# Kernel optimization log

Hardware: AMD Instinct MI355X
Metric: run time of the kernel (lower is better)

Reference implementation:

```python
import jax, jax.numpy as jnp
import numpy as np


def _layernorm(x, g, b, eps=1e-5):
    m = jnp.mean(x, axis=-1, keepdims=True)
    v = jnp.var(x, axis=-1, keepdims=True)
    return (x - m) * jax.lax.rsqrt(v + eps) * g + b


def setup_inputs() -> dict:
    B, S, D, NS = 2, 1024, 1024, 2
    key = jax.random.key(0)
    ks = jax.random.split(key, 20)
    w = lambda k, shape: (jax.random.normal(k, shape, dtype=jnp.float32) * 0.02)
    return {
        "id_x": jax.random.normal(ks[0], (B, S, D), dtype=jnp.float32),
        "side": jax.random.normal(ks[1], (B, S, NS, D), dtype=jnp.float32),
        "num_heads": 16,
        "Wq": w(ks[2], (D, D)), "bq": jnp.zeros((D,), jnp.float32),
        "Wk": w(ks[3], (D, D)), "bk": jnp.zeros((D,), jnp.float32),
        "Wv": w(ks[4], (D, D)), "bv": jnp.zeros((D,), jnp.float32),
        "sWq": w(ks[5], (NS, D, D)), "sbq": jnp.zeros((NS, D), jnp.float32),
        "sWk": w(ks[6], (NS, D, D)), "sbk": jnp.zeros((NS, D), jnp.float32),
        "Wo": w(ks[7], (D, D)), "bo": jnp.zeros((D,), jnp.float32),
        "W1": w(ks[8], (D, D)), "b1": jnp.zeros((D,), jnp.float32),
        "W2": w(ks[9], (D, D)), "b2": jnp.zeros((D,), jnp.float32),
        "g1": jnp.ones((D,), jnp.float32), "be1": jnp.zeros((D,), jnp.float32),
        "g2": jnp.ones((D,), jnp.float32), "be2": jnp.zeros((D,), jnp.float32),
    }


def reference(id_x, side, num_heads, Wq, bq, Wk, bk, Wv, bv, sWq, sbq, sWk, sbk,
              Wo, bo, W1, b1, W2, b2, g1, be1, g2, be2):
    B, S, D = id_x.shape
    NS = side.shape[2]
    H = int(num_heads)
    dh = D // H
    scale = 1.0 / np.sqrt(D)  # source scales by sqrt(dim_H), not sqrt(head_dim)

    # id branch QKV: (B,S,H,dh)
    q = (id_x @ Wq + bq).reshape(B, S, H, dh)
    k = (id_x @ Wk + bk).reshape(B, S, H, dh)
    v = (id_x @ Wv + bv).reshape(B, S, H, dh)
    A_id = jax.nn.softmax(jnp.einsum('bqhd,bkhd->bhqk', q, k) * scale, axis=-1)

    # side branches: per-side Q/K projections, (B,S,NS,H,dh)
    sq = (jnp.einsum('bsnd,nde->bsne', side, sWq) + sbq).reshape(B, S, NS, H, dh)
    sk = (jnp.einsum('bsnd,nde->bsne', side, sWk) + sbk).reshape(B, S, NS, H, dh)
    A_side = jax.nn.softmax(
        jnp.einsum('bqnhd,bknhd->bnhqk', sq, sk) * scale, axis=-1)

    # fuse branches via elementwise max over (1+NS) attention maps
    A = jnp.max(jnp.concatenate([A_id[:, None], A_side], axis=1), axis=1)  # (B,H,q,k)

    O = jnp.einsum('bhqk,bkhd->bqhd', A, v).reshape(B, S, D)
    x = id_x + (O @ Wo + bo)          # residual + fc_o
    x = _layernorm(x, g1, be1)        # ln_mha (post-LN)

    # FF block with exact-erf gelu and residual
    h = jax.nn.gelu(x @ W1 + b1, approximate=False)
    x = x + (h @ W2 + b2)
    x = _layernorm(x, g2, be2)        # ln_ff
    return x
```

## Files before the change

kernel.cpp:

```cpp
#include <hip/hip_runtime.h>
#include <hip/hip_bf16.h>
#include <stdint.h>

typedef float   f32x4  __attribute__((ext_vector_type(4)));
typedef __bf16  bf16x8 __attribute__((ext_vector_type(8)));
typedef unsigned short u16x4 __attribute__((ext_vector_type(4)));
typedef unsigned short u16x8 __attribute__((ext_vector_type(8)));

__device__ __forceinline__ uint16_t f2b(float x) {
  union { float f; uint32_t u; } c; c.f = x;
  uint32_t u = c.u;
  return (uint16_t)((u + 0x7FFFu + ((u >> 16) & 1u)) >> 16);
}
__device__ __forceinline__ float b2f(uint16_t x) {
  union { uint32_t u; float f; } c; c.u = ((uint32_t)x) << 16;
  return c.f;
}

__device__ __forceinline__ f32x4 mfma32(bf16x8 a, bf16x8 b, f32x4 c) {
  return __builtin_amdgcn_mfma_f32_16x16x32_bf16(a, b, c, 0, 0, 0);
}

#define GLDS16(g, l) __builtin_amdgcn_global_load_lds( \
    (const __attribute__((address_space(1))) void*)(const void*)(g), \
    (__attribute__((address_space(3))) void*)(void*)(l), 16, 0, 0)

#define WAITVM(N) asm volatile("s_waitcnt vmcnt(" #N ")" ::: "memory")
#define WAITLGKM0 asm volatile("s_waitcnt lgkmcnt(0)" ::: "memory")
#define BAR() __builtin_amdgcn_s_barrier()

__global__ __launch_bounds__(256) void wtrans_all(
    const float* __restrict__ W0, const float* __restrict__ W1,
    const float* __restrict__ W2, const float* __restrict__ W3,
    const float* __restrict__ W4, const float* __restrict__ W5,
    const float* __restrict__ W6, const float* __restrict__ W7,
    const float* __restrict__ W8, const float* __restrict__ W9,
    uint16_t* __restrict__ WT,
    const float* __restrict__ bq, const float* __restrict__ bk,
    const float* __restrict__ bv, const float* __restrict__ sbq,
    const float* __restrict__ sbk, float* __restrict__ biasc,
    const float* __restrict__ id_x, const float* __restrict__ side,
    uint16_t* __restrict__ xb, uint16_t* __restrict__ sdb) {
  __shared__ float tl[32][33];
  const int tx = threadIdx.x, ty = threadIdx.y;
  if (blockIdx.z >= 11) {
    size_t zi = blockIdx.z - 11;
    size_t base = ((zi * 1024 + blockIdx.y * 32 + blockIdx.x) * 256
                   + ty * 32 + tx) * 4;
    const float* in; uint16_t* out;
    if (base < 2097152) { in = id_x; out = xb; }
    else { in = side; out = sdb; base -= 2097152; }
    f32x4 v = *(const f32x4*)(in + base);
    u16x4 o;
    o[0] = f2b(v[0]); o[1] = f2b(v[1]); o[2] = f2b(v[2]); o[3] = f2b(v[3]);
    *(u16x4*)(out + base) = o;
    return;
  }
  if (blockIdx.z == 10) {
    int i = (blockIdx.y * 32 + blockIdx.x) * 256 + ty * 32 + tx;
    if (i < 7168) {
      int seg = i >> 10, off = i & 1023;
      float v;
      switch (seg) {
        case 0: v = bq[off]; break;
        case 1: v = bk[off]; break;
        case 2: v = bv[off]; break;
        case 3: v = sbq[off]; break;
        case 4: v = sbk[off]; break;
        case 5: v = sbq[1024 + off]; break;
        default: v = sbk[1024 + off]; break;
      }
      biasc[i] = v;
    }
    return;
  }
  const float* W;
  switch (blockIdx.z) {
    case 0: W = W0; break; case 1: W = W1; break; case 2: W = W2; break;
    case 3: W = W3; break; case 4: W = W4; break; case 5: W = W5; break;
    case 6: W = W6; break; case 7: W = W7; break; case 8: W = W8; break;
    default: W = W9; break;
  }
  uint16_t* dst = WT + (size_t)blockIdx.z * 1048576;
  const int n0 = blockIdx.x * 32, k0 = blockIdx.y * 32;
#pragma unroll
  for (int i = 0; i < 32; i += 8)
    tl[ty + i][tx] = W[(size_t)(k0 + ty + i) * 1024 + n0 + tx];
  __syncthreads();
#pragma unroll
  for (int i = 0; i < 32; i += 8)
    dst[(size_t)(n0 + ty + i) * 1024 + k0 + tx] = f2b(tl[tx][ty + i]);
}

__global__ __launch_bounds__(512) void proj_k(
    const uint16_t* __restrict__ xb, const uint16_t* __restrict__ sdb,
    const uint16_t* __restrict__ WT, const float* __restrict__ biasc,
    uint16_t* __restrict__ qkv, uint16_t* __restrict__ sqk0,
    uint16_t* __restrict__ sqk1, uint16_t* __restrict__ vT) {
  __shared__ uint16_t As[2][8192];
  __shared__ uint16_t Bs[2][8192];
  const int xcd = blockIdx.x & 7, s = blockIdx.x >> 3;
  const uint16_t* A; const uint16_t* BT; const float* bias; uint16_t* C;
  int lda, ldc, bx, by;
  bool dovt = false;
  if (s < 48) {
    bx = xcd * 3 + s % 3; by = s / 3;
    A = xb; lda = 1024; BT = WT; bias = biasc; C = qkv; ldc = 3072;
    dovt = bx >= 16;
  } else if (s < 80) {
    int r = s - 48; bx = xcd * 2 + (r & 1); by = r >> 1;
    A = sdb; lda = 2048; BT = WT + 3145728; bias = biasc + 3072;
    C = sqk0; ldc = 2048;
  } else {
    int r = s - 80; bx = xcd * 2 + (r & 1); by = r >> 1;
    A = sdb + 1024; lda = 2048; BT = WT + 5242880; bias = biasc + 5120;
    C = sqk1; ldc = 2048;
  }
  const int t = threadIdx.x;
  const int lane = t & 63, w = t >> 6;
  const int wr = w >> 1, wc = w & 1;
  const int l15 = lane & 15, g = lane >> 4;
  const int bm0 = by * 128, bn0 = bx * 128;

  const int scol = ((t & 3) ^ ((t >> 3) & 3)) * 8;
  const uint16_t* ga = A  + (size_t)(bm0 + (t >> 2)) * lda  + scol;
  const uint16_t* gb = BT + (size_t)(bn0 + (t >> 2)) * 1024 + scol;
  const int gsw = (g ^ ((l15 >> 1) & 3)) * 8;

#define GSTAGE(bufi, k0) do { \
    GLDS16(ga + (k0),      &As[bufi][t * 8]); \
    GLDS16(ga + (k0) + 32, &As[bufi][4096 + t * 8]); \
    GLDS16(gb + (k0),      &Bs[bufi][t * 8]); \
    GLDS16(gb + (k0) + 32, &Bs[bufi][4096 + t * 8]); } while (0)

  f32x4 acc[2][4] = {};
  GSTAGE(0, 0);
  int cur = 0;
  for (int it = 0; it < 16; it++) {
    if (it < 15) { GSTAGE(cur ^ 1, (it + 1) * 64); WAITVM(4); }
    else WAITVM(0);
    BAR();
#pragma unroll
    for (int hf = 0; hf < 2; hf++) {
      const int ho = hf * 4096;
      bf16x8 af[2], bf[4];
#pragma unroll
      for (int i = 0; i < 2; i++)
        af[i] = *(const bf16x8*)&As[cur][ho + (wr * 32 + i * 16 + l15) * 32 + gsw];
#pragma unroll
      for (int i = 0; i < 4; i++)
        bf[i] = *(const bf16x8*)&Bs[cur][ho + (wc * 64 + i * 16 + l15) * 32 + gsw];
#pragma unroll
      for (int mi = 0; mi < 2; mi++)
#pragma unroll
        for (int ni = 0; ni < 4; ni++)
          acc[mi][ni] = mfma32(af[mi], bf[ni], acc[mi][ni]);
    }
    WAITLGKM0;
    BAR();
    cur ^= 1;
  }
#undef GSTAGE

#pragma unroll
  for (int mi = 0; mi < 2; mi++) {
#pragma unroll
    for (int ni = 0; ni < 4; ni++) {
      const int row0 = bm0 + wr * 32 + mi * 16 + g * 4;
      const int col  = bn0 + wc * 64 + ni * 16 + l15;
      const float bc = bias[col];
      u16x4 ov;
#pragma unroll
      for (int r = 0; r < 4; r++) {
        float v = acc[mi][ni][r] + bc;
        ov[r] = f2b(v);
        C[(size_t)(row0 + r) * ldc + col] = ov[r];
      }
      if (dovt) {
        const int cc = col - 2048, hh = cc >> 6, dd = cc & 63;
        const int bb = row0 >> 10, s0 = row0 & 1023;
        *(u16x4*)&vT[((size_t)((bb * 16 + hh) * 64 + dd)) * 1024 + s0] = ov;
      }
    }
  }
}

enum { EPI_BF16 = 0, EPI_RES = 1, EPI_GELU = 2 };

template<int EPI>
__global__ __launch_bounds__(256) void gemm64_k(
    const uint16_t* __restrict__ A, int lda,
    const uint16_t* __restrict__ BT,
    const float* __restrict__ bias,
    const float* __restrict__ res,
    void* __restrict__ Cv, int ldc) {
  __shared__ uint16_t As[4][4096];
  __shared__ uint16_t Bs[4][4096];
  const int t = threadIdx.x;
  const int lane = t & 63, w = t >> 6;
  const int wr = w >> 1, wc = w & 1;
  const int l15 = lane & 15, g = lane >> 4;
  const int bm0 = blockIdx.y * 64, bn0 = blockIdx.x * 64;

  const int scol = ((t & 3) ^ ((t >> 3) & 3)) * 8;
  const uint16_t* ga = A  + (size_t)(bm0 + (t >> 2)) * lda  + scol;
  const uint16_t* gb = BT + (size_t)(bn0 + (t >> 2)) * 1024 + scol;
  const int gsw = (g ^ ((l15 >> 1) & 3)) * 8;

#define GSTAGE64(bufi, k0) do { \
    GLDS16(ga + (k0),      &As[bufi][t * 8]); \
    GLDS16(ga + (k0) + 32, &As[bufi][2048 + t * 8]); \
    GLDS16(gb + (k0),      &Bs[bufi][t * 8]); \
    GLDS16(gb + (k0) + 32, &Bs[bufi][2048 + t * 8]); } while (0)

  f32x4 acc[2][2] = {};
  GSTAGE64(0, 0);
  GSTAGE64(1, 64);
  int cur = 0;
  for (int it = 0; it < 16; it++) {
    if (it < 14) {
      GSTAGE64((cur + 2) & 3, (it + 2) * 64);
      WAITVM(8);
    } else if (it == 14) {
      WAITVM(4);
    } else {
      WAITVM(0);
    }
    BAR();
#pragma unroll
    for (int hf = 0; hf < 2; hf++) {
      const int ho = hf * 2048;
      bf16x8 af[2], bf[2];
#pragma unroll
      for (int i = 0; i < 2; i++)
        af[i] = *(const bf16x8*)&As[cur][ho + (wr * 32 + i * 16 + l15) * 32 + gsw];
#pragma unroll
      for (int i = 0; i < 2; i++)
        bf[i] = *(const bf16x8*)&Bs[cur][ho + (wc * 32 + i * 16 + l15) * 32 + gsw];
#pragma unroll
      for (int mi = 0; mi < 2; mi++)
#pragma unroll
        for (int ni = 0; ni < 2; ni++)
          acc[mi][ni] = mfma32(af[mi], bf[ni], acc[mi][ni]);
    }
    cur = (cur + 1) & 3;
  }
#undef GSTAGE64

#pragma unroll
  for (int mi = 0; mi < 2; mi++) {
#pragma unroll
    for (int ni = 0; ni < 2; ni++) {
      const int row0 = bm0 + wr * 32 + mi * 16 + g * 4;
      const int col  = bn0 + wc * 32 + ni * 16 + l15;
      const float bc = bias[col];
#pragma unroll
      for (int r = 0; r < 4; r++) {
        float v = acc[mi][ni][r] + bc;
        const size_t idx = (size_t)(row0 + r) * ldc + col;
        if constexpr (EPI == EPI_RES) {
          ((float*)Cv)[idx] = v + res[idx];
        } else if constexpr (EPI == EPI_GELU) {
          float gl = 0.5f * v * (1.0f + erff(v * 0.70710678118654752f));
          ((uint16_t*)Cv)[idx] = f2b(gl);
        } else {
          ((uint16_t*)Cv)[idx] = f2b(v);
        }
      }
    }
  }
}

__global__ __launch_bounds__(512) void attn_z(
    const uint16_t* __restrict__ qkv,
    const uint16_t* __restrict__ sqk0,
    const uint16_t* __restrict__ sqk1,
    float* __restrict__ zp) {
  __shared__ uint16_t Sh[2][6144];
  const int t = threadIdx.x;
  const int lane = t & 63, w = t >> 6;
  const int l15 = lane & 15, g = lane >> 4;
  const int half = t >> 8, th = t & 255;
  const int bid = blockIdx.x;
  const int xcd = bid & 7, idx = bid >> 3;
  const int grp = xcd * 8 + (idx >> 3);
  const int qt = idx & 7;
  const int hb = grp >> 1, kc = grp & 1;
  const int b = hb >> 4, h = hb & 15;
  const int q0 = qt * 128 + w * 16;
  const float scl2 = 0.03125f * 1.44269504088896f;
  const size_t rq = (size_t)(b * 1024 + q0 + l15);

  bf16x8 qf[3][2];
  {
    const uint16_t* p = qkv + rq * 3072 + h * 64 + g * 8;
    qf[0][0] = *(const bf16x8*)p; qf[0][1] = *(const bf16x8*)(p + 32);
    p = sqk0 + rq * 2048 + h * 64 + g * 8;
    qf[1][0] = *(const bf16x8*)p; qf[1][1] = *(const bf16x8*)(p + 32);
    p = sqk1 + rq * 2048 + h * 64 + g * 8;
    qf[2][0] = *(const bf16x8*)p; qf[2][1] = *(const bf16x8*)(p + 32);
  }

  const int p_   = th & 15;
  const int gg_  = (th >> 4) & 3;
  const int hf_  = (th >> 6) & 1;
  const int stq_ = th >> 7;
  const int srow   = (p_ >> 2) * 8 + stq_ * 4 + (p_ & 3) + kc * 512;
  const int kcolel = hf_ * 32 + gg_ * 8;

  const uint16_t* srcA = half
      ? sqk0 + (size_t)b * 1024 * 2048 + 1024 + h * 64 + (size_t)srow * 2048 + kcolel
      : qkv  + (size_t)b * 1024 * 3072 + 1024 + h * 64 + (size_t)srow * 3072 + kcolel;
  const size_t incA = half ? (size_t)32 * 2048 : (size_t)32 * 3072;
  const uint16_t* srcB = sqk1 + (size_t)b * 1024 * 2048 + 1024 + h * 64
                       + (size_t)srow * 2048 + kcolel;
  const int offA = half * 2048 + th * 8;
  const int offB = 4096 + th * 8;

#define STAGEZ(bufi) do { \
    GLDS16(srcA, &Sh[bufi][offA]); \
    if (!half) GLDS16(srcB, &Sh[bufi][offB]); \
    srcA += incA; srcB += 32 * 2048; } while (0)

  float z0 = 0.f, z1 = 0.f, z2 = 0.f;
  STAGEZ(0);
  int cur = 0;
  for (int kt = 0; kt < 16; kt++) {
    if (kt < 15) {
      STAGEZ(cur ^ 1);
      if (!half) WAITVM(2); else WAITVM(1);
    } else WAITVM(0);
    BAR();
#pragma unroll
    for (int st = 0; st < 2; st++) {
      f32x4 c0 = {}, c1 = {}, c2 = {};
      c0 = mfma32(*(const bf16x8*)&Sh[cur][st * 1024 + lane * 8],              qf[0][0], c0);
      c0 = mfma32(*(const bf16x8*)&Sh[cur][st * 1024 + 512 + lane * 8],        qf[0][1], c0);
      c1 = mfma32(*(const bf16x8*)&Sh[cur][2048 + st * 1024 + lane * 8],       qf[1][0], c1);
      c1 = mfma32(*(const bf16x8*)&Sh[cur][2048 + st * 1024 + 512 + lane * 8], qf[1][1], c1);
      c2 = mfma32(*(const bf16x8*)&Sh[cur][4096 + st * 1024 + lane * 8],       qf[2][0], c2);
      c2 = mfma32(*(const bf16x8*)&Sh[cur][4096 + st * 1024 + 512 + lane * 8], qf[2][1], c2);
#pragma unroll
      for (int r = 0; r < 4; r++) {
        z0 += __builtin_amdgcn_exp2f(c0[r] * scl2);
        z1 += __builtin_amdgcn_exp2f(c1[r] * scl2);
        z2 += __builtin_amdgcn_exp2f(c2[r] * scl2);
      }
    }
    WAITLGKM0;
    BAR();
    cur ^= 1;
  }
#undef STAGEZ
  z0 += __shfl_xor(z0, 16, 64); z0 += __shfl_xor(z0, 32, 64);
  z1 += __shfl_xor(z1, 16, 64); z1 += __shfl_xor(z1, 32, 64);
  z2 += __shfl_xor(z2, 16, 64); z2 += __shfl_xor(z2, 32, 64);
  if (lane < 16) {
    const int qi = hb * 1024 + q0 + l15;
    zp[kc * 32768 + qi]          = z0;
    zp[65536 + kc * 32768 + qi]  = z1;
    zp[131072 + kc * 32768 + qi] = z2;
  }
}

__global__ __launch_bounds__(512) void attn_o(
    const uint16_t* __restrict__ qkv,
    const uint16_t* __restrict__ sqk0,
    const uint16_t* __restrict__ sqk1,
    const uint16_t* __restrict__ vT,
    const float* __restrict__ zp,
    uint16_t* __restrict__ op) {
  __shared__ uint16_t Sh[2][8192];
  const int t = threadIdx.x;
  const int lane = t & 63, w = t >> 6;
  const int l15 = lane & 15, g = lane >> 4;
  const int half = t >> 8, th = t & 255;
  const int bid = blockIdx.x;
  const int xcd = bid & 7, idx = bid >> 3;
  const int grp = xcd * 8 + (idx >> 3);
  const int qt = idx & 7;
  const int hb = grp >> 1, kc = grp & 1;
  const int b = hb >> 4, h = hb & 15;
  const int q0 = qt * 128 + w * 16;
  const float scl2 = 0.03125f * 1.44269504088896f;
  const size_t rq = (size_t)(b * 1024 + q0 + l15);

  bf16x8 qf[3][2];
  {
    const uint16_t* p = qkv + rq * 3072 + h * 64 + g * 8;
    qf[0][0] = *(const bf16x8*)p; qf[0][1] = *(const bf16x8*)(p + 32);
    p = sqk0 + rq * 2048 + h * 64 + g * 8;
    qf[1][0] = *(const bf16x8*)p; qf[1][1] = *(const bf16x8*)(p + 32);
    p = sqk1 + rq * 2048 + h * 64 + g * 8;
    qf[2][0] = *(const bf16x8*)p; qf[2][1] = *(const bf16x8*)(p + 32);
  }
  const int qi = hb * 1024 + q0 + l15;
  const float lz0 = __builtin_amdgcn_logf(zp[qi] + zp[qi + 32768]);
  const float lz1 = __builtin_amdgcn_logf(zp[qi + 65536] + zp[qi + 98304]);
  const float lz2 = __builtin_amdgcn_logf(zp[qi + 131072] + zp[qi + 163840]);

  const int p_   = th & 15;
  const int gg_  = (th >> 4) & 3;
  const int hf_  = (th >> 6) & 1;
  const int stq_ = th >> 7;
  const int srow   = (p_ >> 2) * 8 + stq_ * 4 + (p_ & 3) + kc * 512;
  const int kcolel = hf_ * 32 + gg_ * 8;

  const uint16_t* srcA = half
      ? sqk0 + (size_t)b * 1024 * 2048 + 1024 + h * 64 + (size_t)srow * 2048 + kcolel
      : qkv  + (size_t)b * 1024 * 3072 + 1024 + h * 64 + (size_t)srow * 3072 + kcolel;
  const size_t incA = half ? (size_t)32 * 2048 : (size_t)32 * 3072;
  const uint16_t* srcB = half
      ? vT + ((size_t)hb * 64 + (th >> 6) * 16 + p_) * 1024 + kc * 512 + gg_ * 8
      : sqk1 + (size_t)b * 1024 * 2048 + 1024 + h * 64 + (size_t)srow * 2048 + kcolel;
  const size_t incB = half ? (size_t)32 : (size_t)32 * 2048;
  const int offA = half * 2048 + th * 8;
  const int offB = 4096 + half * 2048 + th * 8;

#define STAGEO(bufi) do { \
    GLDS16(srcA, &Sh[bufi][offA]); \
    GLDS16(srcB, &Sh[bufi][offB]); \
    srcA += incA; srcB += incB; } while (0)

  f32x4 accO[4] = {};
  STAGEO(0);
  int cur = 0;
  for (int kt = 0; kt < 16; kt++) {
    if (kt < 15) { STAGEO(cur ^ 1); WAITVM(2); }
    else WAITVM(0);
    BAR();
    u16x8 pu;
#pragma unroll
    for (int sub = 0; sub < 2; sub++) {
      f32x4 c0 = {}, c1 = {}, c2 = {};
      c0 = mfma32(*(const bf16x8*)&Sh[cur][sub * 1024 + lane * 8],              qf[0][0], c0);
      c0 = mfma32(*(const bf16x8*)&Sh[cur][sub * 1024 + 512 + lane * 8],        qf[0][1], c0);
      c1 = mfma32(*(const bf16x8*)&Sh[cur][2048 + sub * 1024 + lane * 8],       qf[1][0], c1);
      c1 = mfma32(*(const bf16x8*)&Sh[cur][2048 + sub * 1024 + 512 + lane * 8], qf[1][1], c1);
      c2 = mfma32(*(const bf16x8*)&Sh[cur][4096 + sub * 1024 + lane * 8],       qf[2][0], c2);
      c2 = mfma32(*(const bf16x8*)&Sh[cur][4096 + sub * 1024 + 512 + lane * 8], qf[2][1], c2);
#pragma unroll
      for (int r = 0; r < 4; r++) {
        float m = fmaxf(fmaxf(c0[r] * scl2 - lz0, c1[r] * scl2 - lz1),
                        c2[r] * scl2 - lz2);
        pu[sub * 4 + r] = f2b(__builtin_amdgcn_exp2f(m));
      }
    }
    const bf16x8 pf = __builtin_bit_cast(bf16x8, pu);
#pragma unroll
    for (int dt = 0; dt < 4; dt++) {
      bf16x8 vf = *(const bf16x8*)&Sh[cur][6144 + dt * 512 + lane * 8];
      accO[dt] = mfma32(vf, pf, accO[dt]);
    }
    WAITLGKM0;
    BAR();
    cur ^= 1;
  }
#undef STAGEO

  uint16_t* ob = op + (size_t)kc * 2097152 + rq * 1024 + h * 64;
#pragma unroll
  for (int dt = 0; dt < 4; dt++) {
    u16x4 o4;
#pragma unroll
    for (int r = 0; r < 4; r++) o4[r] = f2b(accO[dt][r]);
    *(u16x4*)(ob + dt * 16 + g * 4) = o4;
  }
}

__global__ __launch_bounds__(256) void ored_k(const uint16_t* __restrict__ op0,
                                              const uint16_t* __restrict__ op1,
                                              uint16_t* __restrict__ Ob) {
  int i = (blockIdx.x * 256 + threadIdx.x) * 4;
  u16x4 a = *(const u16x4*)(op0 + i);
  u16x4 b = *(const u16x4*)(op1 + i);
  u16x4 o;
#pragma unroll
  for (int j = 0; j < 4; j++) o[j] = f2b(b2f(a[j]) + b2f(b[j]));
  *(u16x4*)(Ob + i) = o;
}

template<int WB>
__global__ __launch_bounds__(256) void ln_k(const float* __restrict__ X,
                                            const float* __restrict__ G,
                                            const float* __restrict__ Bt,
                                            float* __restrict__ Yf,
                                            uint16_t* __restrict__ Yb) {
  const int row = blockIdx.x, t = threadIdx.x;
  const int lane = t & 63, w = t >> 6;
  const size_t base = (size_t)row * 1024 + t * 4;
  f32x4 x = *(const f32x4*)(X + base);
  float s  = x[0] + x[1] + x[2] + x[3];
  float s2 = x[0] * x[0] + x[1] * x[1] + x[2] * x[2] + x[3] * x[3];
#pragma unroll
  for (int o = 1; o < 64; o <<= 1) {
    s  += __shfl_xor(s,  o, 64);
    s2 += __shfl_xor(s2, o, 64);
  }
  __shared__ float red[8];
  if (lane == 0) { red[w] = s; red[4 + w] = s2; }
  __syncthreads();
  s  = red[0] + red[1] + red[2] + red[3];
  s2 = red[4] + red[5] + red[6] + red[7];
  const float mean = s * (1.0f / 1024.0f);
  const float rstd = rsqrtf(s2 * (1.0f / 1024.0f) - mean * mean + 1e-5f);
  f32x4 gv = *(const f32x4*)(G + t * 4);
  f32x4 bv = *(const f32x4*)(Bt + t * 4);
  f32x4 y;
#pragma unroll
  for (int i = 0; i < 4; i++) y[i] = (x[i] - mean) * rstd * gv[i] + bv[i];
  *(f32x4*)(Yf + base) = y;
  if constexpr (WB) {
    u16x4 o;
#pragma unroll
    for (int i = 0; i < 4; i++) o[i] = f2b(y[i]);
    *(u16x4*)(Yb + base) = o;
  }
}

extern "C" void kernel_launch(void* const* d_in, const int* in_sizes, int n_in,
                              void* d_out, int out_size, void* d_ws, size_t ws_size,
                              hipStream_t stream) {
  (void)in_sizes; (void)n_in; (void)out_size;
  const float* id_x = (const float*)d_in[0];
  const float* side = (const float*)d_in[1];
  const float* Wq  = (const float*)d_in[3];
  const float* bq  = (const float*)d_in[4];
  const float* Wk  = (const float*)d_in[5];
  const float* bk  = (const float*)d_in[6];
  const float* Wv  = (const float*)d_in[7];
  const float* bv  = (const float*)d_in[8];
  const float* sWq = (const float*)d_in[9];
  const float* sbq = (const float*)d_in[10];
  const float* sWk = (const float*)d_in[11];
  const float* sbk = (const float*)d_in[12];
  const float* Wo  = (const float*)d_in[13];
  const float* bo  = (const float*)d_in[14];
  const float* W1  = (const float*)d_in[15];
  const float* b1  = (const float*)d_in[16];
  const float* W2  = (const float*)d_in[17];
  const float* b2  = (const float*)d_in[18];
  const float* g1  = (const float*)d_in[19];
  const float* be1 = (const float*)d_in[20];
  const float* g2  = (const float*)d_in[21];
  const float* be2 = (const float*)d_in[22];

  char* ws = (char*)d_ws;
  const size_t oWT   = 0;
  const size_t oBias = 20971520;
  const size_t oZP   = 21000192;
  const size_t oC    = 22179840;
  const size_t oD    = 26374144;
  const size_t oE    = 34762752;
  const size_t total = oE + 33554432;
  if (ws_size < total) return;

  uint16_t* WT    = (uint16_t*)(ws + oWT);
  float*    biasc = (float*)(ws + oBias);
  float*    zp    = (float*)(ws + oZP);
  uint16_t* xb    = (uint16_t*)(ws + oC);
  uint16_t* op0   = (uint16_t*)(ws + oC);
  uint16_t* sdb   = (uint16_t*)(ws + oD);
  uint16_t* Ob    = (uint16_t*)(ws + oD + 4194304);
  char* E = ws + oE;
  uint16_t* qkv  = (uint16_t*)(E);
  uint16_t* sqk0 = (uint16_t*)(E + 12582912);
  uint16_t* sqk1 = (uint16_t*)(E + 20971520);
  uint16_t* vTp  = (uint16_t*)(E + 29360128);
  float*    x1   = (float*)(E);
  float*    x1n  = (float*)(E + 8388608);
  uint16_t* x1nb = (uint16_t*)(E + 16777216);
  uint16_t* hb   = (uint16_t*)(E + 20971520);
  float*    x2   = (float*)(E + 25165824);

  wtrans_all<<<dim3(32, 32, 17), dim3(32, 8), 0, stream>>>(
      Wq, Wk, Wv, sWq, sWk, sWq + 1048576, sWk + 1048576, Wo, W1, W2, WT,
      bq, bk, bv, sbq, sbk, biasc, id_x, side, xb, sdb);

  proj_k<<<896, 512, 0, stream>>>(xb, sdb, WT, biasc, qkv, sqk0, sqk1, vTp);

  attn_z<<<512, 512, 0, stream>>>(qkv, sqk0, sqk1, zp);
  attn_o<<<512, 512, 0, stream>>>(qkv, sqk0, sqk1, vTp, zp, op0);
  ored_k<<<2048, 256, 0, stream>>>(op0, op0 + 2097152, Ob);

  gemm64_k<EPI_RES><<<dim3(16, 32), 256, 0, stream>>>(Ob, 1024, WT + 7340032, bo, id_x, x1, 1024);
  ln_k<1><<<2048, 256, 0, stream>>>(x1, g1, be1, x1n, x1nb);
  gemm64_k<EPI_GELU><<<dim3(16, 32), 256, 0, stream>>>(x1nb, 1024, WT + 8388608, b1, nullptr, hb, 1024);
  gemm64_k<EPI_RES><<<dim3(16, 32), 256, 0, stream>>>(hb, 1024, WT + 9437184, b2, x1n, x2, 1024);
  ln_k<0><<<2048, 256, 0, stream>>>(x2, g2, be2, (float*)d_out, nullptr);
}
```

Before: 159.7 us.

## Triple-buffer attention kernels, retile gemm64 K-loop, skip redundant QKV V store

The attention Z and output kernels move from double to triple buffering in LDS, prefetching two k-tiles ahead so global loads overlap more compute. The 64x64 GEMM switches from a 4-stage 64-wide K pipeline to a 2-stage 128-wide one, with an added barrier after each tile. The QKV epilogue no longer writes the V columns to the row-major output, storing them only in the transposed vT buffer. More LDS per block may lower occupancy, and the extra barrier in the GEMM may expose load latency.

Measured after the change: 162.9 us. 1.02x slower.

```diff
diff --git a/kernel.cpp b/kernel.cpp
--- a/kernel.cpp
+++ b/kernel.cpp
@@ -171,15 +171,15 @@
       const float bc = bias[col];
       u16x4 ov;
 #pragma unroll
-      for (int r = 0; r < 4; r++) {
-        float v = acc[mi][ni][r] + bc;
-        ov[r] = f2b(v);
-        C[(size_t)(row0 + r) * ldc + col] = ov[r];
-      }
+      for (int r = 0; r < 4; r++) ov[r] = f2b(acc[mi][ni][r] + bc);
       if (dovt) {
         const int cc = col - 2048, hh = cc >> 6, dd = cc & 63;
         const int bb = row0 >> 10, s0 = row0 & 1023;
         *(u16x4*)&vT[((size_t)((bb * 16 + hh) * 64 + dd)) * 1024 + s0] = ov;
+      } else {
+#pragma unroll
+        for (int r = 0; r < 4; r++)
+          C[(size_t)(row0 + r) * ldc + col] = ov[r];
       }
     }
   }
@@ -194,8 +194,8 @@
     const float* __restrict__ bias,
     const float* __restrict__ res,
     void* __restrict__ Cv, int ldc) {
-  __shared__ uint16_t As[4][4096];
-  __shared__ uint16_t Bs[4][4096];
+  __shared__ uint16_t As[2][8192];
+  __shared__ uint16_t Bs[2][8192];
   const int t = threadIdx.x;
   const int lane = t & 63, w = t >> 6;
   const int wr = w >> 1, wc = w & 1;
@@ -210,25 +210,22 @@
 #define GSTAGE64(bufi, k0) do { \
     GLDS16(ga + (k0),      &As[bufi][t * 8]); \
     GLDS16(ga + (k0) + 32, &As[bufi][2048 + t * 8]); \
+    GLDS16(ga + (k0) + 64, &As[bufi][4096 + t * 8]); \
+    GLDS16(ga + (k0) + 96, &As[bufi][6144 + t * 8]); \
     GLDS16(gb + (k0),      &Bs[bufi][t * 8]); \
-    GLDS16(gb + (k0) + 32, &Bs[bufi][2048 + t * 8]); } while (0)
+    GLDS16(gb + (k0) + 32, &Bs[bufi][2048 + t * 8]); \
+    GLDS16(gb + (k0) + 64, &Bs[bufi][4096 + t * 8]); \
+    GLDS16(gb + (k0) + 96, &Bs[bufi][6144 + t * 8]); } while (0)
 
   f32x4 acc[2][2] = {};
   GSTAGE64(0, 0);
-  GSTAGE64(1, 64);
   int cur = 0;
-  for (int it = 0; it < 16; it++) {
-    if (it < 14) {
-      GSTAGE64((cur + 2) & 3, (it + 2) * 64);
-      WAITVM(8);
-    } else if (it == 14) {
-      WAITVM(4);
-    } else {
-      WAITVM(0);
-    }
-    BAR();
-#pragma unroll
-    for (int hf = 0; hf < 2; hf++) {
+  for (int it = 0; it < 8; it++) {
+    if (it < 7) { GSTAGE64(cur ^ 1, (it + 1) * 128); WAITVM(8); }
+    else WAITVM(0);
+    BAR();
+#pragma unroll
+    for (int hf = 0; hf < 4; hf++) {
       const int ho = hf * 2048;
       bf16x8 af[2], bf[2];
 #pragma unroll
@@ -243,7 +240,9 @@
         for (int ni = 0; ni < 2; ni++)
           acc[mi][ni] = mfma32(af[mi], bf[ni], acc[mi][ni]);
     }
-    cur = (cur + 1) & 3;
+    WAITLGKM0;
+    BAR();
+    cur ^= 1;
   }
 #undef GSTAGE64
 
@@ -276,7 +275,7 @@
     const uint16_t* __restrict__ sqk0,
     const uint16_t* __restrict__ sqk1,
     float* __restrict__ zp) {
-  __shared__ uint16_t Sh[2][6144];
+  __shared__ uint16_t Sh[3][6144];
   const int t = threadIdx.x;
   const int lane = t & 63, w = t >> 6;
   const int l15 = lane & 15, g = lane >> 4;
@@ -324,12 +323,18 @@
 
   float z0 = 0.f, z1 = 0.f, z2 = 0.f;
   STAGEZ(0);
+  STAGEZ(1);
   int cur = 0;
   for (int kt = 0; kt < 16; kt++) {
-    if (kt < 15) {
-      STAGEZ(cur ^ 1);
+    if (kt < 14) {
+      int pre = cur + 2; if (pre >= 3) pre -= 3;
+      STAGEZ(pre);
+      if (!half) WAITVM(4); else WAITVM(2);
+    } else if (kt == 14) {
       if (!half) WAITVM(2); else WAITVM(1);
-    } else WAITVM(0);
+    } else {
+      WAITVM(0);
+    }
     BAR();
 #pragma unroll
     for (int st = 0; st < 2; st++) {
@@ -349,7 +354,7 @@
     }
     WAITLGKM0;
     BAR();
-    cur ^= 1;
+    cur = (cur + 1 == 3) ? 0 : cur + 1;
   }
 #undef STAGEZ
   z0 += __shfl_xor(z0, 16, 64); z0 += __shfl_xor(z0, 32, 64);
@@ -370,7 +375,7 @@
     const uint16_t* __restrict__ vT,
     const float* __restrict__ zp,
     uint16_t* __restrict__ op) {
-  __shared__ uint16_t Sh[2][8192];
+  __shared__ uint16_t Sh[3][8192];
   const int t = threadIdx.x;
   const int lane = t & 63, w = t >> 6;
   const int l15 = lane & 15, g = lane >> 4;
@@ -424,10 +429,18 @@
 
   f32x4 accO[4] = {};
   STAGEO(0);
+  STAGEO(1);
   int cur = 0;
   for (int kt = 0; kt < 16; kt++) {
-    if (kt < 15) { STAGEO(cur ^ 1); WAITVM(2); }
-    else WAITVM(0);
+    if (kt < 14) {
+      int pre = cur + 2; if (pre >= 3) pre -= 3;
+      STAGEO(pre);
+      WAITVM(4);
+    } else if (kt == 14) {
+      WAITVM(2);
+    } else {
+      WAITVM(0);
+    }
     BAR();
     u16x8 pu;
 #pragma unroll
@@ -454,7 +467,7 @@
     }
     WAITLGKM0;
     BAR();
-    cur ^= 1;
+    cur = (cur + 1 == 3) ? 0 : cur + 1;
   }
 #undef STAGEO
 
```
